# Performance work log

Hardware: AMD Instinct MI355X
Metric: run time of the kernel (lower is better)

The kernel has to match this reference:

```python
import jax, jax.numpy as jnp
import numpy as np

B, L, C, H = 32, 641, 768, 12
MEM = 128  # memory slots K; state token at index K; tokens are causal after that


def _block_mask(L, K):
    # rows i attend to cols j per FusedAttention:
    #  memory rows (i<K): attend to memory+state (j<=K)
    #  state row (i==K): attends to everything
    #  token rows (i>K): attend to memory+state (j<=K) and causally to tokens (K<j<=i)
    i = jnp.arange(L)[:, None]
    j = jnp.arange(L)[None, :]
    mem_rows = (i < K) & (j <= K)
    state_row = (i == K)
    tok_rows = (i > K) & ((j <= K) | ((j > K) & (j <= i)))
    return mem_rows | state_row | tok_rows  # (L, L) bool


def setup_inputs() -> dict:
    key = jax.random.key(0)
    k1, k2, k3 = jax.random.split(key, 3)
    x = jax.random.normal(k1, (B, L, C), dtype=jnp.float32)
    W_attn = jax.random.normal(k2, (C, 3 * C), dtype=jnp.float32) * 0.02
    W_proj = jax.random.normal(k3, (C, C), dtype=jnp.float32) * 0.02
    return {"x": x, "W_attn": W_attn, "W_proj": W_proj, "mem_size": MEM}


def reference(x, W_attn, W_proj, mem_size):
    Bb, Ll, Cc = x.shape
    hd = Cc // H
    qkv = x @ W_attn  # (B, L, 3C)
    q, k, v = jnp.split(qkv, 3, axis=-1)
    # (B, H, L, hd)
    q = q.reshape(Bb, Ll, H, hd).transpose(0, 2, 1, 3)
    k = k.reshape(Bb, Ll, H, hd).transpose(0, 2, 1, 3)
    v = v.reshape(Bb, Ll, H, hd).transpose(0, 2, 1, 3)
    mask = _block_mask(Ll, mem_size)  # (L, L)
    scale = 1.0 / jnp.sqrt(jnp.asarray(hd, dtype=x.dtype))
    att = jnp.einsum("bhqd,bhkd->bhqk", q, k) * scale
    att = jnp.where(mask[None, None, :, :], att, jnp.asarray(-jnp.inf, att.dtype))
    att = jax.nn.softmax(att, axis=-1)
    y = jnp.einsum("bhqk,bhkd->bhqd", att, v)
    y = y.transpose(0, 2, 1, 3).reshape(Bb, Ll, Cc)
    return y @ W_proj
```

## Files before the change

### kernel.cpp

```cpp
#include <hip/hip_runtime.h>
#include <stdint.h>

#define B_SZ 32
#define L_SZ 641
#define C_SZ 768
#define H_SZ 12
#define HD 64
#define MEMK 128
#define M_REAL (B_SZ * L_SZ)
#define M_PAD 20608
#define N_QKV (3 * C_SZ)
#define NQT 11
#define QK_STRIDE 1536
#define VT_STRIDE 648
#define SCL_LOG2E 0.18033688f
#define FIXED_MAX 8.0f

typedef __attribute__((ext_vector_type(8))) short short8;
typedef __attribute__((ext_vector_type(4))) float f32x4;
typedef __attribute__((ext_vector_type(4))) unsigned short ushort4v;

__device__ inline unsigned short f2bf(float x) {
  union { float f; uint32_t u; } v; v.f = x;
  uint32_t r = v.u + 0x7fffu + ((v.u >> 16) & 1u);
  return (unsigned short)(r >> 16);
}
__device__ inline float bf2f(short v) {
  union { float f; uint32_t u; } x; x.u = ((uint32_t)(unsigned short)v) << 16;
  return x.f;
}

__device__ inline void gload_lds16(const void* g, void* l) {
  __builtin_amdgcn_global_load_lds(
      (const __attribute__((address_space(1))) uint32_t*)g,
      (__attribute__((address_space(3))) uint32_t*)l, 16, 0, 0);
}

__global__ __launch_bounds__(256) void k_conv_x(const float* __restrict__ src,
                                                unsigned short* __restrict__ dst,
                                                int n4) {
  int i = blockIdx.x * 256 + threadIdx.x;
  if (i >= n4) return;
  float4 v = *(const float4*)(src + (size_t)i * 4);
  ushort4v o = { f2bf(v.x), f2bf(v.y), f2bf(v.z), f2bf(v.w) };
  *(ushort4v*)(dst + (size_t)i * 4) = o;
}

__global__ __launch_bounds__(256) void k_transpose_bf16(const float* __restrict__ src,
                                                        unsigned short* __restrict__ dst,
                                                        int R, int Ccol,
                                                        float scale, int scale_cmax) {
  __shared__ float tile[32][33];
  int c0 = blockIdx.x * 32, r0 = blockIdx.y * 32;
  int tx = threadIdx.x & 31, ty = threadIdx.x >> 5;
  for (int i = ty; i < 32; i += 8)
    tile[i][tx] = src[(size_t)(r0 + i) * Ccol + c0 + tx];
  __syncthreads();
  float sc = (c0 < scale_cmax) ? scale : 1.0f;
  for (int i = ty; i < 32; i += 8)
    dst[(size_t)(c0 + i) * R + r0 + tx] = f2bf(tile[tx][i] * sc);
}

template <int MODE>
__global__ __launch_bounds__(256) void k_gemm(const short* __restrict__ A,
                                              const short* __restrict__ Bt,
                                              void* __restrict__ Cp,
                                              short* __restrict__ vt,
                                              int Mreal, int N, int K) {
  __shared__ short As[2][128 * 64];
  __shared__ short Bs[2][128 * 64];
  int nwg = gridDim.x;
  int qq = nwg >> 3, rr = nwg & 7;
  int x8 = blockIdx.x & 7, i8 = blockIdx.x >> 3;
  int wg = (x8 < rr ? x8 * (qq + 1) : rr * (qq + 1) + (x8 - rr) * qq) + i8;
  const int tiles_n = N >> 7;
  int tm = wg / tiles_n, tn = wg % tiles_n;
  int m0 = tm << 7, n0 = tn << 7;
  int lane = threadIdx.x & 63, wave = threadIdx.x >> 6;
  int wr = wave >> 1, wc = wave & 1;
  int l15 = lane & 15, g = lane >> 4;

  f32x4 acc[4][4];
  f32x4 z = {0.f, 0.f, 0.f, 0.f};
#pragma unroll
  for (int i = 0; i < 4; ++i)
#pragma unroll
    for (int j = 0; j < 4; ++j) acc[i][j] = z;

  int arow = lane >> 3;
  int acol = (lane & 7) * 8;

#define STAGE(K0, BUF)                                                        \
  {                                                                           \
    _Pragma("unroll")                                                         \
    for (int cc = 0; cc < 4; ++cc) {                                          \
      int rb = (cc * 4 + wave) * 8;                                           \
      gload_lds16(A + (size_t)(m0 + rb + arow) * K + ((K0) + acol),           \
                  (char*)As[BUF] + rb * 128);                                 \
      gload_lds16(Bt + (size_t)(n0 + rb + arow) * K + ((K0) + acol),          \
                  (char*)Bs[BUF] + rb * 128);                                 \
    }                                                                         \
  }

  STAGE(0, 0);
  STAGE(64, 1);
  int nk = K >> 6;
  for (int t = 0; t < nk; ++t) {
    int buf = t & 1;
    if (t + 1 < nk) {
      asm volatile("s_waitcnt vmcnt(8)" ::: "memory");
    } else {
      asm volatile("s_waitcnt vmcnt(0)" ::: "memory");
    }
    __builtin_amdgcn_s_barrier();
#pragma unroll
    for (int ks = 0; ks < 2; ++ks) {
      short8 a[4], b[4];
      if (MODE == 3) {
#pragma unroll
        for (int nf = 0; nf < 4; ++nf)
          a[nf] = *(const short8*)&Bs[buf][(wr * 64 + nf * 16 + l15) * 64 + ks * 32 + g * 8];
#pragma unroll
        for (int mf = 0; mf < 4; ++mf)
          b[mf] = *(const short8*)&As[buf][(wc * 64 + mf * 16 + l15) * 64 + ks * 32 + g * 8];
      } else {
#pragma unroll
        for (int mf = 0; mf < 4; ++mf)
          a[mf] = *(const short8*)&As[buf][(wr * 64 + mf * 16 + l15) * 64 + ks * 32 + g * 8];
#pragma unroll
        for (int nf = 0; nf < 4; ++nf)
          b[nf] = *(const short8*)&Bs[buf][(wc * 64 + nf * 16 + l15) * 64 + ks * 32 + g * 8];
      }
#pragma unroll
      for (int i = 0; i < 4; ++i)
#pragma unroll
        for (int j = 0; j < 4; ++j)
          acc[i][j] = __builtin_amdgcn_mfma_f32_16x16x32_bf16(a[i], b[j], acc[i][j], 0, 0, 0);
    }
    __builtin_amdgcn_s_barrier();
    __builtin_amdgcn_sched_barrier(0);
    if (t + 2 < nk) STAGE((t + 2) << 6, buf);
  }
#undef STAGE

  if (MODE == 3) {
#pragma unroll
    for (int nf = 0; nf < 4; ++nf) {
#pragma unroll
      for (int reg = 0; reg < 4; ++reg) {
        int n = n0 + wr * 64 + nf * 16 + g * 4 + reg;
        int h = n >> 6, d = n & 63;
        int xr = (d & 7) << 3;
#pragma unroll
        for (int mf = 0; mf < 4; ++mf) {
          int m = m0 + wc * 64 + mf * 16 + l15;
          if (m >= Mreal) continue;
          int bb = (unsigned)m / 641u;
          int key = m - bb * 641;
          int k2 = (key >= 640) ? key : (key ^ xr);
          vt[((size_t)(bb * H_SZ + h) * HD + d) * VT_STRIDE + k2] = f2bf(acc[nf][mf][reg]);
        }
      }
    }
    return;
  }
#pragma unroll
  for (int mf = 0; mf < 4; ++mf) {
#pragma unroll
    for (int reg = 0; reg < 4; ++reg) {
      int m = m0 + wr * 64 + mf * 16 + g * 4 + reg;
      if (m >= Mreal) continue;
      int xr = 0;
      if (MODE == 2) {
        int bb = (unsigned)m / 641u;
        int key = m - bb * 641;
        xr = (key & 7) << 3;
      }
#pragma unroll
      for (int nf = 0; nf < 4; ++nf) {
        int n = n0 + wc * 64 + nf * 16 + l15;
        float v = acc[mf][nf][reg];
        if (MODE == 2) {
          int nn = (n >= C_SZ) ? (n ^ xr) : n;
          ((unsigned short*)Cp)[(size_t)m * QK_STRIDE + nn] = f2bf(v);
        } else
          ((float*)Cp)[(size_t)m * N + n] = v;
      }
    }
  }
}

__global__ __launch_bounds__(256) void k_attn(const short* __restrict__ qk,
                                              const short* __restrict__ vt,
                                              short* __restrict__ y) {
  __shared__ short Ks[2][64 * 64];
  __shared__ short Vt[2][64 * 64];
  __shared__ short Ps[4][16 * 64];

  int bid = blockIdx.x;
  int work = (bid & 7) * 528 + (bid >> 3);
  int qt = work % NQT;
  int rem = work / NQT;
  int h = rem % H_SZ;
  int b = rem / H_SZ;
  int q0 = qt * 64;
  int lane = threadIdx.x & 63, w = threadIdx.x >> 6;
  int l15 = lane & 15, g = lane >> 4;

  size_t qbase = (size_t)(b * L_SZ + q0 + w * 16 + l15) * QK_STRIDE + h * HD;
  short8 qa[2];
#pragma unroll
  for (int ks = 0; ks < 2; ++ks)
    qa[ks] = *(const short8*)&qk[qbase + ks * 32 + g * 8];

  f32x4 o[4];
  float l_run[4];
  f32x4 z = {0.f, 0.f, 0.f, 0.f};
  f32x4 m8 = {-FIXED_MAX, -FIXED_MAX, -FIXED_MAX, -FIXED_MAX};
#pragma unroll
  for (int df = 0; df < 4; ++df) o[df] = z;
#pragma unroll
  for (int r = 0; r < 4; ++r) l_run[r] = 0.f;

  int jmax[4];
#pragma unroll
  for (int reg = 0; reg < 4; ++reg) {
    int i = q0 + w * 16 + g * 4 + reg;
    jmax[reg] = (i == MEMK) ? (L_SZ - 1) : (i < MEMK ? MEMK : i);
  }
  int imin = q0 + w * 16;
  int jm_min = (imin <= MEMK) ? MEMK : imin;

  int q1 = q0 + 63; if (q1 > L_SZ - 1) q1 = L_SZ - 1;
  int col_max = (q0 <= MEMK && MEMK <= q1) ? (L_SZ - 1) : (q1 < MEMK ? MEMK : q1);

  size_t kbase = (size_t)b * L_SZ * QK_STRIDE + C_SZ + h * HD;
  size_t vbase = (size_t)(b * H_SZ + h) * HD * VT_STRIDE;

  int i0 = threadIdx.x >> 3, j0e = (threadIdx.x & 7) * 8;
  int i1 = (threadIdx.x + 256) >> 3, j1e = j0e;
  int rswz = (l15 & 7) << 4;

#define STAGE_ATTN(C0, BUF)                                                   \
  {                                                                           \
    gload_lds16(qk + kbase + (size_t)((C0) + i0) * QK_STRIDE + j0e,           \
                (char*)Ks[BUF] + w * 1024);                                   \
    gload_lds16(qk + kbase + (size_t)((C0) + i1) * QK_STRIDE + j1e,           \
                (char*)Ks[BUF] + w * 1024 + 4096);                            \
    gload_lds16(vt + vbase + (size_t)i0 * VT_STRIDE + (C0) + j0e,             \
                (char*)Vt[BUF] + w * 1024);                                   \
    gload_lds16(vt + vbase + (size_t)i1 * VT_STRIDE + (C0) + j1e,             \
                (char*)Vt[BUF] + w * 1024 + 4096);                            \
  }

  STAGE_ATTN(0, 0);

  int nt = col_max >> 6;
  for (int t = 0; t <= nt; ++t) {
    int c0 = t << 6;
    int buf = t & 1;
    __syncthreads();
    if (t < nt) STAGE_ATTN(c0 + 64, buf ^ 1);
    int vswz = (c0 >= 640) ? 0 : rswz;

    f32x4 s[4];
#pragma unroll
    for (int kf = 0; kf < 4; ++kf) {
      f32x4 sa = m8;
#pragma unroll
      for (int ks = 0; ks < 2; ++ks) {
        short8 kb = *(const short8*)((char*)Ks[buf] +
                        (kf * 16 + l15) * 128 + ((ks * 64 + g * 16) ^ rswz));
        sa = __builtin_amdgcn_mfma_f32_16x16x32_bf16(qa[ks], kb, sa, 0, 0, 0);
      }
      s[kf] = sa;
    }

    if (c0 + 63 > jm_min) {
#pragma unroll
      for (int kf = 0; kf < 4; ++kf) {
        int j = c0 + kf * 16 + l15;
#pragma unroll
        for (int reg = 0; reg < 4; ++reg)
          s[kf][reg] = (j <= jmax[reg]) ? s[kf][reg] : -1e30f;
      }
    }

#pragma unroll
    for (int kf = 0; kf < 4; ++kf)
#pragma unroll
      for (int reg = 0; reg < 4; ++reg)
        s[kf][reg] = exp2f(s[kf][reg]);
#pragma unroll
    for (int reg = 0; reg < 4; ++reg)
      l_run[reg] += (s[0][reg] + s[1][reg]) + (s[2][reg] + s[3][reg]);

#pragma unroll
    for (int reg = 0; reg < 4; ++reg) {
      int q = g * 4 + reg;
      char* prow = (char*)Ps[w] + q * 128;
      int qswz = (q & 7) << 4;
#pragma unroll
      for (int kf = 0; kf < 4; kf += 2) {
        uint32_t r;
        asm("v_cvt_pk_bf16_f32 %0, %1, %2"
            : "=v"(r) : "v"(s[kf][reg]), "v"(s[kf + 1][reg]));
        *(short*)(prow + ((kf * 32 + l15 * 2) ^ qswz)) = (short)(r & 0xffff);
        *(short*)(prow + (((kf + 1) * 32 + l15 * 2) ^ qswz)) = (short)(r >> 16);
      }
    }

    short8 pa[2];
#pragma unroll
    for (int ks = 0; ks < 2; ++ks)
      pa[ks] = *(const short8*)((char*)Ps[w] + l15 * 128 + ((ks * 64 + g * 16) ^ rswz));
#pragma unroll
    for (int df = 0; df < 4; ++df) {
#pragma unroll
      for (int ks = 0; ks < 2; ++ks) {
        short8 vb = *(const short8*)((char*)Vt[buf] +
                        (df * 16 + l15) * 128 + ((ks * 64 + g * 16) ^ vswz));
        o[df] = __builtin_amdgcn_mfma_f32_16x16x32_bf16(pa[ks], vb, o[df], 0, 0, 0);
      }
    }
  }
#undef STAGE_ATTN

#pragma unroll
  for (int reg = 0; reg < 4; ++reg) {
    float ls = l_run[reg];
    ls += __shfl_xor(ls, 1);
    ls += __shfl_xor(ls, 2);
    ls += __shfl_xor(ls, 4);
    ls += __shfl_xor(ls, 8);
    int i = q0 + w * 16 + g * 4 + reg;
    if (i >= L_SZ) continue;
    float inv = 1.0f / ls;
#pragma unroll
    for (int df = 0; df < 4; ++df)
      y[(size_t)(b * L_SZ + i) * C_SZ + h * HD + df * 16 + l15] = (short)f2bf(o[df][reg] * inv);
  }
}

extern "C" void kernel_launch(void* const* d_in, const int* in_sizes, int n_in,
                              void* d_out, int out_size, void* d_ws, size_t ws_size,
                              hipStream_t stream) {
  const float* x = (const float*)d_in[0];
  const float* Wa = (const float*)d_in[1];
  const float* Wp = (const float*)d_in[2];
  float* out = (float*)d_out;

  char* ws = (char*)d_ws;
  size_t off0 = 0;
  short* x_bf = (short*)(ws + off0);
  size_t off1 = off0 + (size_t)M_PAD * C_SZ * 2;
  short* Wa_t = (short*)(ws + off1);
  size_t off2 = off1 + (size_t)N_QKV * C_SZ * 2;
  short* Wp_t = (short*)(ws + off2);
  size_t off3 = off2 + (size_t)C_SZ * C_SZ * 2;
  short* qk = (short*)(ws + off3);
  size_t off4 = off3 + (size_t)M_REAL * QK_STRIDE * 2;
  short* vt = (short*)(ws + off4);
  size_t need = off4 + (size_t)B_SZ * H_SZ * HD * VT_STRIDE * 2 + 4096;
  if (ws_size < need) return;

  int n4 = M_REAL * C_SZ / 4;
  k_conv_x<<<(n4 + 255) / 256, 256, 0, stream>>>(x, (unsigned short*)x_bf, n4);
  k_transpose_bf16<<<dim3(N_QKV / 32, C_SZ / 32), 256, 0, stream>>>(
      Wa, (unsigned short*)Wa_t, C_SZ, N_QKV, SCL_LOG2E, C_SZ);
  k_transpose_bf16<<<dim3(C_SZ / 32, C_SZ / 32), 256, 0, stream>>>(
      Wp, (unsigned short*)Wp_t, C_SZ, C_SZ, 1.0f, 0);

  k_gemm<2><<<(M_PAD / 128) * (QK_STRIDE / 128), 256, 0, stream>>>(
      x_bf, Wa_t, (void*)qk, nullptr, M_REAL, QK_STRIDE, C_SZ);
  k_gemm<3><<<(M_PAD / 128) * (C_SZ / 128), 256, 0, stream>>>(
      x_bf, Wa_t + (size_t)QK_STRIDE * C_SZ, nullptr, vt, M_REAL, C_SZ, C_SZ);
  k_attn<<<B_SZ * H_SZ * NQT, 256, 0, stream>>>(qk, vt, x_bf );
  k_gemm<0><<<(M_PAD / 128) * (C_SZ / 128), 256, 0, stream>>>(
      x_bf, Wp_t, (void*)out, nullptr, M_REAL, C_SZ, C_SZ);
}
```

Before: 261.9 us.

## Process 128 query rows per attention block with 8 waves sharing K/V tiles

The attention kernel now uses 512-thread blocks that each cover 128 query rows (two 64-row groups) instead of 64, so every staged K/V tile in LDS is reused by twice as many waves and the grid shrinks from 11 to 6 query tiles per head. Each thread stages one 16-byte chunk per tile instead of two. Waves whose rows lie past the end or whose causal range is finished skip the compute but still take part in staging and barriers. The cost is uneven work inside a block: in causal blocks the lower waves sit idle while the upper ones finish, and there are fewer, larger blocks to spread across the GPU.

```diff
diff --git a/kernel.cpp b/kernel.cpp
--- a/kernel.cpp
+++ b/kernel.cpp
@@ -10,7 +10,7 @@
 #define M_REAL (B_SZ * L_SZ)
 #define M_PAD 20608
 #define N_QKV (3 * C_SZ)
-#define NQT 11
+#define NQP 6
 #define QK_STRIDE 1536
 #define VT_STRIDE 648
 #define SCL_LOG2E 0.18033688f
@@ -190,24 +190,27 @@
   }
 }
 
-__global__ __launch_bounds__(256) void k_attn(const short* __restrict__ qk,
+__global__ __launch_bounds__(512) void k_attn(const short* __restrict__ qk,
                                               const short* __restrict__ vt,
                                               short* __restrict__ y) {
   __shared__ short Ks[2][64 * 64];
   __shared__ short Vt[2][64 * 64];
-  __shared__ short Ps[4][16 * 64];
+  __shared__ short Ps[8][16 * 64];
 
   int bid = blockIdx.x;
-  int work = (bid & 7) * 528 + (bid >> 3);
-  int qt = work % NQT;
-  int rem = work / NQT;
+  int work = (bid & 7) * 288 + (bid >> 3);
+  int qp = work % NQP;
+  int rem = work / NQP;
   int h = rem % H_SZ;
   int b = rem / H_SZ;
-  int q0 = qt * 64;
-  int lane = threadIdx.x & 63, w = threadIdx.x >> 6;
+  int q0 = qp * 128;
+  int tid = threadIdx.x;
+  int lane = tid & 63, w = tid >> 6;
+  int wgp = w >> 2;
   int l15 = lane & 15, g = lane >> 4;
-
-  size_t qbase = (size_t)(b * L_SZ + q0 + w * 16 + l15) * QK_STRIDE + h * HD;
+  int q0w = q0 + wgp * 64 + (w & 3) * 16;
+
+  size_t qbase = (size_t)(b * L_SZ + q0w + l15) * QK_STRIDE + h * HD;
   short8 qa[2];
 #pragma unroll
   for (int ks = 0; ks < 2; ++ks)
@@ -225,32 +228,30 @@
   int jmax[4];
 #pragma unroll
   for (int reg = 0; reg < 4; ++reg) {
-    int i = q0 + w * 16 + g * 4 + reg;
+    int i = q0w + g * 4 + reg;
     jmax[reg] = (i == MEMK) ? (L_SZ - 1) : (i < MEMK ? MEMK : i);
   }
-  int imin = q0 + w * 16;
-  int jm_min = (imin <= MEMK) ? MEMK : imin;
-
-  int q1 = q0 + 63; if (q1 > L_SZ - 1) q1 = L_SZ - 1;
+  int jm_min = (q0w <= MEMK) ? MEMK : q0w;
+
+  int q1 = q0 + 127; if (q1 > L_SZ - 1) q1 = L_SZ - 1;
   int col_max = (q0 <= MEMK && MEMK <= q1) ? (L_SZ - 1) : (q1 < MEMK ? MEMK : q1);
+  int qw1 = q0w + 15;
+  bool dead = (q0w >= L_SZ);
+  int wcol = (q0w <= MEMK && MEMK <= qw1) ? (L_SZ - 1) : (qw1 < MEMK ? MEMK : qw1);
+  if (dead) wcol = -1;
 
   size_t kbase = (size_t)b * L_SZ * QK_STRIDE + C_SZ + h * HD;
   size_t vbase = (size_t)(b * H_SZ + h) * HD * VT_STRIDE;
 
-  int i0 = threadIdx.x >> 3, j0e = (threadIdx.x & 7) * 8;
-  int i1 = (threadIdx.x + 256) >> 3, j1e = j0e;
+  int i0 = tid >> 3, j0e = (tid & 7) * 8;
   int rswz = (l15 & 7) << 4;
 
 #define STAGE_ATTN(C0, BUF)                                                   \
   {                                                                           \
     gload_lds16(qk + kbase + (size_t)((C0) + i0) * QK_STRIDE + j0e,           \
                 (char*)Ks[BUF] + w * 1024);                                   \
-    gload_lds16(qk + kbase + (size_t)((C0) + i1) * QK_STRIDE + j1e,           \
-                (char*)Ks[BUF] + w * 1024 + 4096);                            \
     gload_lds16(vt + vbase + (size_t)i0 * VT_STRIDE + (C0) + j0e,             \
                 (char*)Vt[BUF] + w * 1024);                                   \
-    gload_lds16(vt + vbase + (size_t)i1 * VT_STRIDE + (C0) + j1e,             \
-                (char*)Vt[BUF] + w * 1024 + 4096);                            \
   }
 
   STAGE_ATTN(0, 0);
@@ -261,6 +262,7 @@
     int buf = t & 1;
     __syncthreads();
     if (t < nt) STAGE_ATTN(c0 + 64, buf ^ 1);
+    if (c0 > wcol) continue;
     int vswz = (c0 >= 640) ? 0 : rswz;
 
     f32x4 s[4];
@@ -333,7 +335,7 @@
     ls += __shfl_xor(ls, 2);
     ls += __shfl_xor(ls, 4);
     ls += __shfl_xor(ls, 8);
-    int i = q0 + w * 16 + g * 4 + reg;
+    int i = q0w + g * 4 + reg;
     if (i >= L_SZ) continue;
     float inv = 1.0f / ls;
 #pragma unroll
@@ -375,7 +377,7 @@
       x_bf, Wa_t, (void*)qk, nullptr, M_REAL, QK_STRIDE, C_SZ);
   k_gemm<3><<<(M_PAD / 128) * (C_SZ / 128), 256, 0, stream>>>(
       x_bf, Wa_t + (size_t)QK_STRIDE * C_SZ, nullptr, vt, M_REAL, C_SZ, C_SZ);
-  k_attn<<<B_SZ * H_SZ * NQT, 256, 0, stream>>>(qk, vt, x_bf );
+  k_attn<<<B_SZ * H_SZ * NQP, 512, 0, stream>>>(qk, vt, x_bf );
   k_gemm<0><<<(M_PAD / 128) * (C_SZ / 128), 256, 0, stream>>>(
       x_bf, Wp_t, (void*)out, nullptr, M_REAL, C_SZ, C_SZ);
 }
```

After: 259.1 us. About the same (-1.1%).
